# Performance work log

Hardware: AMD Instinct MI355X
Metric: run time of the kernel (lower is better)

The kernel has to match this reference:

```python
import jax, jax.numpy as jnp
import numpy as np

N_NODES = 100000
N_EDGES = 1000000
IN_DIM = 128
HID = 128
OUT_DIM = 40


def setup_inputs() -> dict:
    key = jax.random.key(0)
    ks = jax.random.split(key, 16)
    x = jax.random.normal(ks[0], (N_NODES, IN_DIM), dtype=jnp.float32)
    edge_index = jax.random.randint(ks[1], (2, N_EDGES), 0, N_NODES, dtype=jnp.int64)
    s = 0.05
    # GAT layer 1 (in->hid, heads=1, concat=True)
    W1 = jax.random.normal(ks[2], (HID, IN_DIM), jnp.float32) * s
    b1 = jnp.zeros((HID,), jnp.float32)
    att1 = jax.random.normal(ks[3], (1, 2 * HID), jnp.float32) * s
    bias1 = jnp.zeros((HID,), jnp.float32)
    # GAT layer 2 (hid->hid)
    W2 = jax.random.normal(ks[4], (HID, HID), jnp.float32) * s
    b2 = jnp.zeros((HID,), jnp.float32)
    att2 = jax.random.normal(ks[5], (1, 2 * HID), jnp.float32) * s
    bias2 = jnp.zeros((HID,), jnp.float32)
    # post_mp: Linear(hid,hid) -> Dropout -> Linear(hid,out)
    Wp1 = jax.random.normal(ks[6], (HID, HID), jnp.float32) * s
    bp1 = jnp.zeros((HID,), jnp.float32)
    Wp2 = jax.random.normal(ks[7], (OUT_DIM, HID), jnp.float32) * s
    bp2 = jnp.zeros((OUT_DIM,), jnp.float32)
    return dict(x=x, edge_index=edge_index, W1=W1, b1=b1, att1=att1, bias1=bias1,
                W2=W2, b2=b2, att2=att2, bias2=bias2,
                Wp1=Wp1, bp1=bp1, Wp2=Wp2, bp2=bp2)


def gat_layer(x, src, dst, W, b, att, bias, n_nodes):
    # x: [N, Fin] -> h: [N, C] (heads=1, concat=True)
    h = x @ W.T + b
    C = h.shape[1]
    att_i, att_j = att[0, :C], att[0, C:]  # split: first half pairs with x_i (dst), second with x_j (src)
    # per-node scalar projections, then gather per edge (avoids [E,2C] concat)
    e = (h @ att_i)[dst] + (h @ att_j)[src]  # [E]
    e = jnp.where(e > 0, e, 0.2 * e)  # leaky_relu(0.2)
    # segment softmax over destination nodes
    m = jax.ops.segment_max(e, dst, num_segments=n_nodes)
    ex = jnp.exp(e - m[dst])
    denom = jax.ops.segment_sum(ex, dst, num_segments=n_nodes)
    alpha = ex / denom[dst]
    out = jax.ops.segment_sum(h[src] * alpha[:, None], dst, num_segments=n_nodes)
    return out + bias


def reference(x, edge_index, W1, b1, att1, bias1, W2, b2, att2, bias2, Wp1, bp1, Wp2, bp2):
    src, dst = edge_index[0], edge_index[1]
    n = x.shape[0]
    h = jax.nn.relu(gat_layer(x, src, dst, W1, b1, att1, bias1, n))  # dropout p=0 -> identity
    h = jax.nn.relu(gat_layer(h, src, dst, W2, b2, att2, bias2, n))
    y = (h @ Wp1.T + bp1) @ Wp2.T + bp2  # post_mp (eval: dropout identity)
    return jax.nn.log_softmax(y, axis=1)
```

## Files before the change

kernel.cpp:

```cpp
#include <hip/hip_runtime.h>

#define N_NODES 100000
#define N_EDGES 1000000
#define HID 128
#define OUT_DIM 40
#define CSR_W 64
#define CUR_STRIDE 16
#define GEMM_TILES 1563
#define G2_TILES 782
#define PROJ_TILES 1563
#define EDGE_BLK 977
#define WC_BLK 21

typedef __attribute__((ext_vector_type(8))) short bf16x8;
typedef __attribute__((ext_vector_type(4))) float f32x4;
typedef __attribute__((ext_vector_type(2))) float f32x2;

__device__ inline unsigned short f2bf(float f) {
    unsigned u = __float_as_uint(f);
    u += 0x7fffu + ((u >> 16) & 1u);
    return (unsigned short)(u >> 16);
}
__device__ inline float bf2f(unsigned short u) {
    return __uint_as_float(((unsigned)u) << 16);
}

#if __has_builtin(__builtin_amdgcn_cvt_pk_f32_fp8) && __has_builtin(__builtin_amdgcn_cvt_pk_fp8_f32)
#define HAVE_HW_FP8 1
#endif

__device__ inline f32x2 fp8x2_to_f32(unsigned short u) {
#ifdef HAVE_HW_FP8
    return __builtin_amdgcn_cvt_pk_f32_fp8((int)(unsigned)u, false);
#else
    f32x2 r;
    unsigned v0 = u & 0xFF, v1 = (u >> 8) & 0xFF;
    unsigned m0 = v0 & 0x7F, m1 = v1 & 0x7F;
    float a0 = (m0 >= 8) ? __uint_as_float((m0 << 20) + 0x3C000000) : (float)m0 * (1.f/512.f);
    float a1 = (m1 >= 8) ? __uint_as_float((m1 << 20) + 0x3C000000) : (float)m1 * (1.f/512.f);
    r.x = (v0 & 0x80) ? -a0 : a0;
    r.y = (v1 & 0x80) ? -a1 : a1;
    return r;
#endif
}

__device__ inline unsigned char f32_to_fp8(float f) {
#ifdef HAVE_HW_FP8
    return (unsigned char)(__builtin_amdgcn_cvt_pk_fp8_f32(f, 0.f, 0u, false) & 0xFF);
#else
    float a = fabsf(f);
    unsigned s = (__float_as_uint(f) >> 31) << 7;
    if (a >= 448.f) return (unsigned char)(s | 0x7E);
    if (a < 0.015625f) {
        int q = (int)rintf(a * 512.f);
        return (unsigned char)(s | q);
    }
    unsigned u = __float_as_uint(a);
    u += 0x7FFFFu + ((u >> 20) & 1u);
    int be = (int)(u >> 23) - 120;
    unsigned m = (u >> 20) & 7;
    if (be >= 16) return (unsigned char)(s | 0x7E);
    if (be <= 0) { int q = (int)rintf(a * 512.f); return (unsigned char)(s | q); }
    return (unsigned char)(s | (be << 3) | m);
#endif
}

__device__ inline float4 ld4(const float* p) { return *(const float4*)p; }
__device__ inline float4 ld4(const unsigned short* p) {
    ushort4 u = *(const ushort4*)p;
    return make_float4(bf2f(u.x), bf2f(u.y), bf2f(u.z), bf2f(u.w));
}

__global__ __launch_bounds__(256) void zero_kernel(float4* __restrict__ p, int n4) {
    int i = blockIdx.x * 256 + threadIdx.x;
    int stride = gridDim.x * 256;
    float4 z = make_float4(0.f, 0.f, 0.f, 0.f);
    for (; i < n4; i += stride) p[i] = z;
}

#define LDA 136
template<typename AT>
__device__ __forceinline__ void gemm_tile_body(
    int tile, const AT* __restrict__ A, const float* __restrict__ W,
    const float* __restrict__ out_bias, const float* __restrict__ in_bias,
    int relu_in, const float* __restrict__ att,
    unsigned char* __restrict__ Cb8, float* __restrict__ hi, float2* __restrict__ hjsc,
    int n_rows, unsigned short* As, unsigned short* Ws)
{
    const int t = threadIdx.x;
    const int row0 = tile * 64;

    for (int i = 0; i < 8; i++) {
        int lin = t + i * 256;
        int r = lin >> 5;
        int k = (lin & 31) * 4;
        int gr = row0 + r;
        float4 av = make_float4(0.f, 0.f, 0.f, 0.f);
        if (gr < n_rows) av = ld4(A + (size_t)gr * HID + k);
        if (in_bias) {
            av.x += in_bias[k + 0]; av.y += in_bias[k + 1];
            av.z += in_bias[k + 2]; av.w += in_bias[k + 3];
            if (relu_in) {
                av.x = fmaxf(av.x, 0.f); av.y = fmaxf(av.y, 0.f);
                av.z = fmaxf(av.z, 0.f); av.w = fmaxf(av.w, 0.f);
            }
        }
        ushort4 bv;
        bv.x = f2bf(av.x); bv.y = f2bf(av.y); bv.z = f2bf(av.z); bv.w = f2bf(av.w);
        *(ushort4*)(&As[r * LDA + k]) = bv;
    }
    for (int i = 0; i < 16; i++) {
        int lin = t + i * 256;
        int r = lin >> 5;
        int k = (lin & 31) * 4;
        float4 wv = *(const float4*)(W + (size_t)r * HID + k);
        ushort4 bv;
        bv.x = f2bf(wv.x); bv.y = f2bf(wv.y); bv.z = f2bf(wv.z); bv.w = f2bf(wv.w);
        *(ushort4*)(&Ws[r * LDA + k]) = bv;
    }
    __syncthreads();

    const int wave = t >> 6, lane = t & 63;
    const int lrow = lane & 15, quad = lane >> 4;
    const int wrow = wave * 16;

    f32x4 acc[8];
    #pragma unroll
    for (int ni = 0; ni < 8; ni++) acc[ni] = (f32x4){0.f, 0.f, 0.f, 0.f};

    #pragma unroll
    for (int ks = 0; ks < 4; ks++) {
        const int kb = ks * 32 + quad * 8;
        bf16x8 af = *(bf16x8*)(&As[(wrow + lrow) * LDA + kb]);
        #pragma unroll
        for (int ni = 0; ni < 8; ni++) {
            bf16x8 bfr = *(bf16x8*)(&Ws[(ni * 16 + lrow) * LDA + kb]);
            acc[ni] = __builtin_amdgcn_mfma_f32_16x16x32_bf16(af, bfr, acc[ni], 0, 0, 0);
        }
    }

    float pi[4] = {0.f, 0.f, 0.f, 0.f}, pj[4] = {0.f, 0.f, 0.f, 0.f};
    float amax[4] = {0.f, 0.f, 0.f, 0.f};
    const int rbase = row0 + wrow + quad * 4;
    #pragma unroll
    for (int ni = 0; ni < 8; ni++) {
        const int col = ni * 16 + lrow;
        const float bo = out_bias[col];
        const float ai = att[col], aj = att[HID + col];
        #pragma unroll
        for (int r = 0; r < 4; r++) {
            float v = acc[ni][r] + bo;
            amax[r] = fmaxf(amax[r], fabsf(v));
            pi[r] = fmaf(v, ai, pi[r]);
            pj[r] = fmaf(v, aj, pj[r]);
        }
    }
    #pragma unroll
    for (int o = 1; o < 16; o <<= 1) {
        #pragma unroll
        for (int r = 0; r < 4; r++) {
            amax[r] = fmaxf(amax[r], __shfl_xor(amax[r], o));
            pi[r] += __shfl_xor(pi[r], o);
            pj[r] += __shfl_xor(pj[r], o);
        }
    }
    float inv[4], scl[4];
    #pragma unroll
    for (int r = 0; r < 4; r++) {
        float a = fmaxf(amax[r], 1e-20f);
        scl[r] = a * (1.f / 448.f);
        inv[r] = 448.f / a;
    }
    #pragma unroll
    for (int ni = 0; ni < 8; ni++) {
        const int col = ni * 16 + lrow;
        const float bo = out_bias[col];
        #pragma unroll
        for (int r = 0; r < 4; r++) {
            int gr = rbase + r;
            if (gr < n_rows)
                Cb8[(size_t)gr * HID + col] = f32_to_fp8((acc[ni][r] + bo) * inv[r]);
        }
    }
    if (lrow == 0) {
        #pragma unroll
        for (int r = 0; r < 4; r++) {
            int gr = rbase + r;
            if (gr < n_rows) { hi[gr] = pi[r]; hjsc[gr] = make_float2(pj[r], scl[r]); }
        }
    }
}

__global__ __launch_bounds__(256) void combined_prep(
    const float* __restrict__ x, const float* __restrict__ W1,
    const float* __restrict__ b1, const float* __restrict__ att1,
    const float* __restrict__ Wp1, const float* __restrict__ bp1,
    const float* __restrict__ Wp2, const float* __restrict__ bp2,
    const int* __restrict__ src, const int* __restrict__ dst,
    unsigned* __restrict__ cursor, int* __restrict__ csr,
    unsigned char* __restrict__ hb8, float* __restrict__ hi, float2* __restrict__ hjsc,
    float* __restrict__ Wc, float* __restrict__ bc)
{
    __shared__ unsigned short As[64 * LDA];
    __shared__ unsigned short Ws[128 * LDA];
    const int b = blockIdx.x, g = b >> 3, r = b & 7;

    if (r < 3) {
        const int eid = g * 3 + r;
        if (eid >= EDGE_BLK) return;
        int e = eid * 1024 + threadIdx.x;
        #pragma unroll
        for (int j = 0; j < 4; j++, e += 256) {
            if (e < N_EDGES) {
                int d = dst[e], s = src[e];
                unsigned p = atomicAdd(&cursor[d << 4], 1u);
                if (p < CSR_W) __builtin_nontemporal_store(s, &csr[(d << 6) + p]);
            }
        }
        return;
    }
    const int oid = g * 5 + (r - 3);
    if (oid < WC_BLK) {
        int t = oid * 256 + threadIdx.x;
        if (t < OUT_DIM * HID) {
            int o = t >> 7, k = t & 127;
            float s = 0.f;
            for (int j = 0; j < HID; j++) s = fmaf(Wp2[o * HID + j], Wp1[j * HID + k], s);
            Wc[t] = s;
        } else if (t < OUT_DIM * HID + OUT_DIM) {
            int o = t - OUT_DIM * HID;
            float s = bp2[o];
            for (int j = 0; j < HID; j++) s = fmaf(Wp2[o * HID + j], bp1[j], s);
            bc[o] = s;
        }
        return;
    }
    const int tile = oid - WC_BLK;
    if (tile >= GEMM_TILES) return;
    gemm_tile_body<float>(tile, x, W1, b1, nullptr, 0, att1, hb8, hi, hjsc, N_NODES, As, Ws);
}

__global__ __launch_bounds__(256) void gemm_mfma_b128(
    const unsigned short* __restrict__ A, const float* __restrict__ W,
    const float* __restrict__ out_bias, const float* __restrict__ in_bias,
    const float* __restrict__ att,
    unsigned char* __restrict__ Cb8, float* __restrict__ hi, float2* __restrict__ hjsc,
    int n_rows)
{
    __shared__ unsigned short As[128 * LDA];
    __shared__ unsigned short Ws[128 * LDA];
    const int t = threadIdx.x;
    const int row0 = blockIdx.x * 128;

    for (int i = 0; i < 16; i++) {
        int lin = t + i * 256;
        int r = lin >> 5;
        int k = (lin & 31) * 4;
        int gr = row0 + r;
        float4 av = make_float4(0.f, 0.f, 0.f, 0.f);
        if (gr < n_rows) av = ld4(A + (size_t)gr * HID + k);
        av.x = fmaxf(av.x + in_bias[k + 0], 0.f);
        av.y = fmaxf(av.y + in_bias[k + 1], 0.f);
        av.z = fmaxf(av.z + in_bias[k + 2], 0.f);
        av.w = fmaxf(av.w + in_bias[k + 3], 0.f);
        ushort4 bv;
        bv.x = f2bf(av.x); bv.y = f2bf(av.y); bv.z = f2bf(av.z); bv.w = f2bf(av.w);
        *(ushort4*)(&As[r * LDA + k]) = bv;
    }
    for (int i = 0; i < 16; i++) {
        int lin = t + i * 256;
        int r = lin >> 5;
        int k = (lin & 31) * 4;
        float4 wv = *(const float4*)(W + (size_t)r * HID + k);
        ushort4 bv;
        bv.x = f2bf(wv.x); bv.y = f2bf(wv.y); bv.z = f2bf(wv.z); bv.w = f2bf(wv.w);
        *(ushort4*)(&Ws[r * LDA + k]) = bv;
    }
    __syncthreads();

    const int wave = t >> 6, lane = t & 63;
    const int lrow = lane & 15, quad = lane >> 4;

    f32x4 acc[2][8];
    #pragma unroll
    for (int mt = 0; mt < 2; mt++)
        #pragma unroll
        for (int ni = 0; ni < 8; ni++) acc[mt][ni] = (f32x4){0.f, 0.f, 0.f, 0.f};

    #pragma unroll
    for (int ks = 0; ks < 4; ks++) {
        const int kb = ks * 32 + quad * 8;
        bf16x8 af0 = *(bf16x8*)(&As[(wave * 32 + lrow) * LDA + kb]);
        bf16x8 af1 = *(bf16x8*)(&As[(wave * 32 + 16 + lrow) * LDA + kb]);
        #pragma unroll
        for (int ni = 0; ni < 8; ni++) {
            bf16x8 bfr = *(bf16x8*)(&Ws[(ni * 16 + lrow) * LDA + kb]);
            acc[0][ni] = __builtin_amdgcn_mfma_f32_16x16x32_bf16(af0, bfr, acc[0][ni], 0, 0, 0);
            acc[1][ni] = __builtin_amdgcn_mfma_f32_16x16x32_bf16(af1, bfr, acc[1][ni], 0, 0, 0);
        }
    }

    #pragma unroll
    for (int mt = 0; mt < 2; mt++) {
        float pi[4] = {0.f, 0.f, 0.f, 0.f}, pj[4] = {0.f, 0.f, 0.f, 0.f};
        float amax[4] = {0.f, 0.f, 0.f, 0.f};
        const int rbase = row0 + wave * 32 + mt * 16 + quad * 4;
        #pragma unroll
        for (int ni = 0; ni < 8; ni++) {
            const int col = ni * 16 + lrow;
            const float bo = out_bias[col];
            const float ai = att[col], aj = att[HID + col];
            #pragma unroll
            for (int r = 0; r < 4; r++) {
                float v = acc[mt][ni][r] + bo;
                amax[r] = fmaxf(amax[r], fabsf(v));
                pi[r] = fmaf(v, ai, pi[r]);
                pj[r] = fmaf(v, aj, pj[r]);
            }
        }
        #pragma unroll
        for (int o = 1; o < 16; o <<= 1) {
            #pragma unroll
            for (int r = 0; r < 4; r++) {
                amax[r] = fmaxf(amax[r], __shfl_xor(amax[r], o));
                pi[r] += __shfl_xor(pi[r], o);
                pj[r] += __shfl_xor(pj[r], o);
            }
        }
        float inv[4], scl[4];
        #pragma unroll
        for (int r = 0; r < 4; r++) {
            float a = fmaxf(amax[r], 1e-20f);
            scl[r] = a * (1.f / 448.f);
            inv[r] = 448.f / a;
        }
        #pragma unroll
        for (int ni = 0; ni < 8; ni++) {
            const int col = ni * 16 + lrow;
            const float bo = out_bias[col];
            #pragma unroll
            for (int r = 0; r < 4; r++) {
                int gr = rbase + r;
                if (gr < n_rows)
                    Cb8[(size_t)gr * HID + col] = f32_to_fp8((acc[mt][ni][r] + bo) * inv[r]);
            }
        }
        if (lrow == 0) {
            #pragma unroll
            for (int r = 0; r < 4; r++) {
                int gr = rbase + r;
                if (gr < n_rows) { hi[gr] = pi[r]; hjsc[gr] = make_float2(pj[r], scl[r]); }
            }
        }
    }
}

__global__ __launch_bounds__(256) void fused_gat(
    const unsigned* __restrict__ cursor, const int* __restrict__ csr,
    const unsigned char* __restrict__ hb8,
    const float* __restrict__ hi, const float2* __restrict__ hjsc,
    unsigned short* __restrict__ out)
{
    const int wave = threadIdx.x >> 6;
    const int lane = threadIdx.x & 63;
    const int d = blockIdx.x * 4 + wave;
    if (d >= N_NODES) return;
    unsigned deg = cursor[d << 4];
    if (deg > CSR_W) deg = CSR_W;
    const int cnt = (int)deg;
    const float hid = hi[d];
    const int base = d << 6;

    int sv = 0;
    float ev = -INFINITY, esc = 0.f;
    if (lane < cnt) {
        sv = csr[base + lane];
        float2 gg = hjsc[sv];
        float e = hid + gg.x;
        ev = e > 0.f ? e : 0.2f * e;
        esc = gg.y;
    }
    float m = ev;
    #pragma unroll
    for (int o = 32; o; o >>= 1) m = fmaxf(m, __shfl_xor(m, o));
    const float exv = (lane < cnt) ? __expf(ev - m) : 0.f;
    float denom = exv;
    #pragma unroll
    for (int o = 32; o; o >>= 1) denom += __shfl_xor(denom, o);
    const float wv = exv * esc;

    float accx = 0.f, accy = 0.f;
    const int co = lane * 2;
    int i = 0;
    for (; i + 4 <= cnt; i += 4) {
        const int s0 = __shfl(sv, i),     s1 = __shfl(sv, i + 1);
        const int s2 = __shfl(sv, i + 2), s3 = __shfl(sv, i + 3);
        const float w0 = __shfl(wv, i),     w1 = __shfl(wv, i + 1);
        const float w2 = __shfl(wv, i + 2), w3 = __shfl(wv, i + 3);
        const unsigned short u0 = *(const unsigned short*)(hb8 + (size_t)s0 * HID + co);
        const unsigned short u1 = *(const unsigned short*)(hb8 + (size_t)s1 * HID + co);
        const unsigned short u2 = *(const unsigned short*)(hb8 + (size_t)s2 * HID + co);
        const unsigned short u3 = *(const unsigned short*)(hb8 + (size_t)s3 * HID + co);
        const f32x2 f0 = fp8x2_to_f32(u0);
        const f32x2 f1 = fp8x2_to_f32(u1);
        const f32x2 f2 = fp8x2_to_f32(u2);
        const f32x2 f3 = fp8x2_to_f32(u3);
        accx = fmaf(w0, f0.x, accx); accy = fmaf(w0, f0.y, accy);
        accx = fmaf(w1, f1.x, accx); accy = fmaf(w1, f1.y, accy);
        accx = fmaf(w2, f2.x, accx); accy = fmaf(w2, f2.y, accy);
        accx = fmaf(w3, f3.x, accx); accy = fmaf(w3, f3.y, accy);
    }
    for (; i < cnt; i++) {
        const int s = __shfl(sv, i);
        const float w = __shfl(wv, i);
        const unsigned short u = *(const unsigned short*)(hb8 + (size_t)s * HID + co);
        const f32x2 f = fp8x2_to_f32(u);
        accx = fmaf(w, f.x, accx);
        accy = fmaf(w, f.y, accy);
    }
    const float inv = cnt ? 1.f / denom : 0.f;
    ushort2 o2;
    o2.x = f2bf(accx * inv);
    o2.y = f2bf(accy * inv);
    *(ushort2*)(out + (size_t)d * HID + co) = o2;
}

__global__ __launch_bounds__(256) void final_proj_mfma(
    const unsigned short* __restrict__ agg, const float* __restrict__ bias2,
    const float* __restrict__ Wc, const float* __restrict__ bc,
    float* __restrict__ out)
{
    __shared__ unsigned short As[64 * LDA];
    __shared__ unsigned short Ws[48 * LDA];
    const int t = threadIdx.x;
    const int node0 = blockIdx.x * 64;

    for (int i = 0; i < 5; i++) {
        int lin = t + i * 256;
        int r = lin >> 5;
        int k = (lin & 31) * 4;
        float4 wv = *(const float4*)(Wc + (size_t)r * HID + k);
        ushort4 bv;
        bv.x = f2bf(wv.x); bv.y = f2bf(wv.y); bv.z = f2bf(wv.z); bv.w = f2bf(wv.w);
        *(ushort4*)(&Ws[r * LDA + k]) = bv;
    }
    {
        int r = 40 + (t >> 5);
        int k = (t & 31) * 4;
        ushort4 z; z.x = 0; z.y = 0; z.z = 0; z.w = 0;
        *(ushort4*)(&Ws[r * LDA + k]) = z;
    }
    for (int i = 0; i < 8; i++) {
        int lin = t + i * 256;
        int r = lin >> 5;
        int k = (lin & 31) * 4;
        int gr = node0 + r;
        float4 v = make_float4(0.f, 0.f, 0.f, 0.f);
        if (gr < N_NODES) v = ld4(agg + (size_t)gr * HID + k);
        v.x = fmaxf(v.x + bias2[k + 0], 0.f);
        v.y = fmaxf(v.y + bias2[k + 1], 0.f);
        v.z = fmaxf(v.z + bias2[k + 2], 0.f);
        v.w = fmaxf(v.w + bias2[k + 3], 0.f);
        ushort4 bv;
        bv.x = f2bf(v.x); bv.y = f2bf(v.y); bv.z = f2bf(v.z); bv.w = f2bf(v.w);
        *(ushort4*)(&As[r * LDA + k]) = bv;
    }
    __syncthreads();

    const int wave = t >> 6, lane = t & 63;
    const int lrow = lane & 15, quad = lane >> 4;
    const int wrow = wave * 16;

    f32x4 acc[3];
    #pragma unroll
    for (int nt = 0; nt < 3; nt++) acc[nt] = (f32x4){0.f, 0.f, 0.f, 0.f};

    #pragma unroll
    for (int ks = 0; ks < 4; ks++) {
        const int kb = ks * 32 + quad * 8;
        bf16x8 af = *(bf16x8*)(&As[(wrow + lrow) * LDA + kb]);
        #pragma unroll
        for (int nt = 0; nt < 3; nt++) {
            bf16x8 bfr = *(bf16x8*)(&Ws[(nt * 16 + lrow) * LDA + kb]);
            acc[nt] = __builtin_amdgcn_mfma_f32_16x16x32_bf16(af, bfr, acc[nt], 0, 0, 0);
        }
    }

    int cols[3]; float bcv[3]; bool valid[3];
    #pragma unroll
    for (int nt = 0; nt < 3; nt++) {
        cols[nt] = nt * 16 + lrow;
        valid[nt] = cols[nt] < OUT_DIM;
        bcv[nt] = valid[nt] ? bc[cols[nt]] : 0.f;
    }
    const int rbase = node0 + wrow + quad * 4;
    #pragma unroll
    for (int r = 0; r < 4; r++) {
        float v[3];
        float mx = -INFINITY;
        #pragma unroll
        for (int nt = 0; nt < 3; nt++) {
            v[nt] = acc[nt][r] + bcv[nt];
            if (valid[nt]) mx = fmaxf(mx, v[nt]);
        }
        #pragma unroll
        for (int o = 1; o < 16; o <<= 1) mx = fmaxf(mx, __shfl_xor(mx, o));
        float s = 0.f;
        #pragma unroll
        for (int nt = 0; nt < 3; nt++)
            if (valid[nt]) s += __expf(v[nt] - mx);
        #pragma unroll
        for (int o = 1; o < 16; o <<= 1) s += __shfl_xor(s, o);
        const float lse = mx + __logf(s);
        const int node = rbase + r;
        if (node < N_NODES) {
            #pragma unroll
            for (int nt = 0; nt < 3; nt++)
                if (valid[nt]) out[(size_t)node * OUT_DIM + cols[nt]] = v[nt] - lse;
        }
    }
}

extern "C" void kernel_launch(void* const* d_in, const int* in_sizes, int n_in,
                              void* d_out, int out_size, void* d_ws, size_t ws_size,
                              hipStream_t stream)
{
    const float* x     = (const float*)d_in[0];
    const int*   ei    = (const int*)d_in[1];
    const float* W1    = (const float*)d_in[2];
    const float* b1    = (const float*)d_in[3];
    const float* att1  = (const float*)d_in[4];
    const float* bias1 = (const float*)d_in[5];
    const float* W2    = (const float*)d_in[6];
    const float* b2    = (const float*)d_in[7];
    const float* att2  = (const float*)d_in[8];
    const float* bias2 = (const float*)d_in[9];
    const float* Wp1   = (const float*)d_in[10];
    const float* bp1   = (const float*)d_in[11];
    const float* Wp2   = (const float*)d_in[12];
    const float* bp2   = (const float*)d_in[13];
    float* out = (float*)d_out;

    const int* src = ei;
    const int* dst = ei + N_EDGES;

    char* ws = (char*)d_ws;
    unsigned char* hb8   = (unsigned char*)ws;
    unsigned short* aggb = (unsigned short*)(ws + (size_t)N_NODES * HID);
    float* hi      = (float*)(aggb + (size_t)N_NODES * HID);
    float2* hjsc   = (float2*)(hi + N_NODES);
    unsigned* cursor = (unsigned*)(hjsc + N_NODES);
    int* csr       = (int*)(cursor + (size_t)N_NODES * CUR_STRIDE);
    float* Wc      = (float*)(csr + (size_t)N_NODES * CSR_W);
    float* bc      = Wc + OUT_DIM * HID;

    const int prep_blocks = 326 * 8;

    zero_kernel<<<512, 256, 0, stream>>>((float4*)cursor, N_NODES * CUR_STRIDE / 4);

    combined_prep<<<prep_blocks, 256, 0, stream>>>(
        x, W1, b1, att1, Wp1, bp1, Wp2, bp2, src, dst,
        cursor, csr, hb8, hi, hjsc, Wc, bc);

    fused_gat<<<N_NODES / 4, 256, 0, stream>>>(cursor, csr, hb8, hi, hjsc, aggb);

    gemm_mfma_b128<<<G2_TILES, 256, 0, stream>>>(aggb, W2, b2, bias1, att2, hb8, hi, hjsc, N_NODES);
    fused_gat<<<N_NODES / 4, 256, 0, stream>>>(cursor, csr, hb8, hi, hjsc, aggb);

    final_proj_mfma<<<PROJ_TILES, 256, 0, stream>>>(aggb, bias2, Wc, bc, out);
}
```

Before: 319.8 us.

## Fuse second GAT aggregation into final projection kernel; use memset for cursor

The second-layer GAT aggregation now runs inside the final projection kernel. Each wave aggregates 16 nodes and writes the bias+relu bf16 rows straight into shared memory before the MFMA projection. This removes the write and re-read of the aggregated hidden buffer and one kernel launch. The trade-off is fewer waves in flight for the gather phase (1563 blocks each doing 64 nodes serially per wave), which may reduce latency hiding. The zero kernel is also replaced with hipMemsetAsync.

```diff
diff --git a/kernel.cpp b/kernel.cpp
--- a/kernel.cpp
+++ b/kernel.cpp
@@ -8,7 +8,7 @@
 #define CUR_STRIDE 16
 #define GEMM_TILES 1563
 #define G2_TILES 782
-#define PROJ_TILES 1563
+#define GP_TILES 1563
 #define EDGE_BLK 977
 #define WC_BLK 21
 
@@ -69,13 +69,6 @@
 __device__ inline float4 ld4(const unsigned short* p) {
     ushort4 u = *(const ushort4*)p;
     return make_float4(bf2f(u.x), bf2f(u.y), bf2f(u.z), bf2f(u.w));
-}
-
-__global__ __launch_bounds__(256) void zero_kernel(float4* __restrict__ p, int n4) {
-    int i = blockIdx.x * 256 + threadIdx.x;
-    int stride = gridDim.x * 256;
-    float4 z = make_float4(0.f, 0.f, 0.f, 0.f);
-    for (; i < n4; i += stride) p[i] = z;
 }
 
 #define LDA 136
@@ -355,16 +348,12 @@
     }
 }
 
-__global__ __launch_bounds__(256) void fused_gat(
-    const unsigned* __restrict__ cursor, const int* __restrict__ csr,
+__device__ __forceinline__ void gat_node(
+    int d, const unsigned* __restrict__ cursor, const int* __restrict__ csr,
     const unsigned char* __restrict__ hb8,
     const float* __restrict__ hi, const float2* __restrict__ hjsc,
-    unsigned short* __restrict__ out)
-{
-    const int wave = threadIdx.x >> 6;
-    const int lane = threadIdx.x & 63;
-    const int d = blockIdx.x * 4 + wave;
-    if (d >= N_NODES) return;
+    int lane, float& accx, float& accy, float& inv)
+{
     unsigned deg = cursor[d << 4];
     if (deg > CSR_W) deg = CSR_W;
     const int cnt = (int)deg;
@@ -389,7 +378,7 @@
     for (int o = 32; o; o >>= 1) denom += __shfl_xor(denom, o);
     const float wv = exv * esc;
 
-    float accx = 0.f, accy = 0.f;
+    accx = 0.f; accy = 0.f;
     const int co = lane * 2;
     int i = 0;
     for (; i + 4 <= cnt; i += 4) {
@@ -418,15 +407,32 @@
         accx = fmaf(w, f.x, accx);
         accy = fmaf(w, f.y, accy);
     }
-    const float inv = cnt ? 1.f / denom : 0.f;
+    inv = cnt ? 1.f / denom : 0.f;
+}
+
+__global__ __launch_bounds__(256) void fused_gat(
+    const unsigned* __restrict__ cursor, const int* __restrict__ csr,
+    const unsigned char* __restrict__ hb8,
+    const float* __restrict__ hi, const float2* __restrict__ hjsc,
+    unsigned short* __restrict__ out)
+{
+    const int wave = threadIdx.x >> 6;
+    const int lane = threadIdx.x & 63;
+    const int d = blockIdx.x * 4 + wave;
+    if (d >= N_NODES) return;
+    float accx, accy, inv;
+    gat_node(d, cursor, csr, hb8, hi, hjsc, lane, accx, accy, inv);
     ushort2 o2;
     o2.x = f2bf(accx * inv);
     o2.y = f2bf(accy * inv);
-    *(ushort2*)(out + (size_t)d * HID + co) = o2;
-}
-
-__global__ __launch_bounds__(256) void final_proj_mfma(
-    const unsigned short* __restrict__ agg, const float* __restrict__ bias2,
+    *(ushort2*)(out + (size_t)d * HID + lane * 2) = o2;
+}
+
+__global__ __launch_bounds__(256) void gat_proj(
+    const unsigned* __restrict__ cursor, const int* __restrict__ csr,
+    const unsigned char* __restrict__ hb8,
+    const float* __restrict__ hi, const float2* __restrict__ hjsc,
+    const float* __restrict__ bias2,
     const float* __restrict__ Wc, const float* __restrict__ bc,
     float* __restrict__ out)
 {
@@ -434,6 +440,7 @@
     __shared__ unsigned short Ws[48 * LDA];
     const int t = threadIdx.x;
     const int node0 = blockIdx.x * 64;
+    const int wave = t >> 6, lane = t & 63;
 
     for (int i = 0; i < 5; i++) {
         int lin = t + i * 256;
@@ -450,24 +457,22 @@
         ushort4 z; z.x = 0; z.y = 0; z.z = 0; z.w = 0;
         *(ushort4*)(&Ws[r * LDA + k]) = z;
     }
-    for (int i = 0; i < 8; i++) {
-        int lin = t + i * 256;
-        int r = lin >> 5;
-        int k = (lin & 31) * 4;
-        int gr = node0 + r;
-        float4 v = make_float4(0.f, 0.f, 0.f, 0.f);
-        if (gr < N_NODES) v = ld4(agg + (size_t)gr * HID + k);
-        v.x = fmaxf(v.x + bias2[k + 0], 0.f);
-        v.y = fmaxf(v.y + bias2[k + 1], 0.f);
-        v.z = fmaxf(v.z + bias2[k + 2], 0.f);
-        v.w = fmaxf(v.w + bias2[k + 3], 0.f);
-        ushort4 bv;
-        bv.x = f2bf(v.x); bv.y = f2bf(v.y); bv.z = f2bf(v.z); bv.w = f2bf(v.w);
-        *(ushort4*)(&As[r * LDA + k]) = bv;
+
+    const int co = lane * 2;
+    const float b2x = bias2[co], b2y = bias2[co + 1];
+    for (int s = 0; s < 16; s++) {
+        const int lr = wave * 16 + s;
+        const int d = node0 + lr;
+        float accx = 0.f, accy = 0.f, inv = 0.f;
+        if (d < N_NODES)
+            gat_node(d, cursor, csr, hb8, hi, hjsc, lane, accx, accy, inv);
+        ushort2 o2;
+        o2.x = f2bf(fmaxf(accx * inv + b2x, 0.f));
+        o2.y = f2bf(fmaxf(accy * inv + b2y, 0.f));
+        *(ushort2*)(&As[lr * LDA + co]) = o2;
     }
     __syncthreads();
 
-    const int wave = t >> 6, lane = t & 63;
     const int lrow = lane & 15, quad = lane >> 4;
     const int wrow = wave * 16;
 
@@ -556,7 +561,7 @@
 
     const int prep_blocks = 326 * 8;
 
-    zero_kernel<<<512, 256, 0, stream>>>((float4*)cursor, N_NODES * CUR_STRIDE / 4);
+    hipMemsetAsync(cursor, 0, (size_t)N_NODES * CUR_STRIDE * sizeof(unsigned), stream);
 
     combined_prep<<<prep_blocks, 256, 0, stream>>>(
         x, W1, b1, att1, Wp1, bp1, Wp2, bp2, src, dst,
@@ -565,7 +570,6 @@
     fused_gat<<<N_NODES / 4, 256, 0, stream>>>(cursor, csr, hb8, hi, hjsc, aggb);
 
     gemm_mfma_b128<<<G2_TILES, 256, 0, stream>>>(aggb, W2, b2, bias1, att2, hb8, hi, hjsc, N_NODES);
-    fused_gat<<<N_NODES / 4, 256, 0, stream>>>(cursor, csr, hb8, hi, hjsc, aggb);
-
-    final_proj_mfma<<<PROJ_TILES, 256, 0, stream>>>(aggb, bias2, Wc, bc, out);
-}
+
+    gat_proj<<<GP_TILES, 256, 0, stream>>>(cursor, csr, hb8, hi, hjsc, bias2, Wc, bc, out);
+}
```

New measurement: 350.0 us. 1.09x slower.
